# Performance work log

Hardware: AMD Instinct MI355X
Metric: run time of the kernel (lower is better)

Reference implementation:

```python
import jax, jax.numpy as jnp
import numpy as np

THRESHOLD_IOU = 0.8  # forward default in the original module


def setup_inputs() -> dict:
    key = jax.random.key(0)
    k1, k2, k3, k4 = jax.random.split(key, 4)
    N = M = 16
    H = W = 768
    # Binary masks (the original zeroes pixels to 0.0 and tests >0 via torch.where)
    masks_a = (jax.random.uniform(k1, (N, H, W)) > 0.6).astype(jnp.float32)
    masks_b = (jax.random.uniform(k2, (M, H, W)) > 0.6).astype(jnp.float32)
    # Make a few masks identical across labels so the IoU>threshold (suppression)
    # branch is exercised, not just the partial-overlap zeroing branch.
    masks_b = masks_b.at[:4].set(masks_a[:4])
    scores_a = jax.random.uniform(k3, (N,))
    scores_b = jax.random.uniform(k4, (M,))
    return {"masks_a": masks_a, "masks_b": masks_b,
            "scores_a": scores_a, "scores_b": scores_b}


def _overlap_filter(masks_a, masks_b, scores_a, scores_b, thr):
    # Sequential pairwise IoU + overlap zeroing, faithful to the original
    # nested product(enumerate(masks), enumerate(other_masks)) loop order
    # (i outer, j inner), where each pair sees masks already modified by
    # earlier pairs. Pruning ("keep") is applied after the loop; here it is
    # represented with static shapes as keep flags + zeroed-out rows.
    N, H, W = masks_a.shape
    M = masks_b.shape[0]
    P = H * W
    A0 = masks_a.reshape(N, P)
    B0 = masks_b.reshape(M, P)

    def body(carry, k):
        A, B, fi, fj = carry
        i = k // M
        j = k % M
        a = A[i]  # [P]
        b = B[j]  # [P]
        abin = a > 0
        bbin = b > 0
        inter = abin & bbin
        inter_sum = jnp.sum(inter.astype(jnp.float32))
        union_sum = jnp.sum((abin | bbin).astype(jnp.float32))
        iou = inter_sum / jnp.maximum(union_sum, 1.0)
        a_wins = scores_a[i] > scores_b[j]
        suppress = iou > thr                 # mark whole loser mask for removal
        zero_case = (iou > 0) & ~suppress    # zero overlapped pixels of loser
        b_new = jnp.where(zero_case & a_wins & inter, 0.0, b)
        a_new = jnp.where(zero_case & (~a_wins) & inter, 0.0, a)
        A = A.at[i].set(a_new)
        B = B.at[j].set(b_new)
        fj = fj.at[j].set(fj[j] | (suppress & a_wins))
        fi = fi.at[i].set(fi[i] | (suppress & ~a_wins))
        return (A, B, fi, fj), None

    fi0 = jnp.zeros(N, dtype=bool)
    fj0 = jnp.zeros(M, dtype=bool)
    (A, B, fi, fj), _ = jax.lax.scan(body, (A0, B0, fi0, fj0), jnp.arange(N * M))
    keep_a = ~fi
    keep_b = ~fj
    A = jnp.where(keep_a[:, None], A, 0.0)
    B = jnp.where(keep_b[:, None], B, 0.0)
    return A.reshape(N, H, W), B.reshape(M, H, W), keep_a, keep_b


def reference(masks_a, masks_b, scores_a, scores_b):
    return _overlap_filter(masks_a, masks_b, scores_a, scores_b, THRESHOLD_IOU)
```

## Files before the change

kernel.cpp:

```cpp
#include <hip/hip_runtime.h>
#include <stdint.h>

#define NM 16
#define HW_P 589824
#define U8PM 9216
#define F4PM 147456
#define F4PT 2359296
#define PT 512
#define NG 8

typedef unsigned long long u64;
typedef float vf4 __attribute__((ext_vector_type(4)));


__device__ __forceinline__ uint32_t spread4(uint32_t x) {
    uint32_t t = (x | (x << 12)) & 0x000F000Fu;
    t = (t | (t << 6)) & 0x03030303u;
    t = (t | (t << 3)) & 0x11111111u;
    return t;
}

__global__ __launch_bounds__(256) void binarize_kernel(
    const float* __restrict__ ma, const float* __restrict__ mb,
    uint32_t* __restrict__ bitsA, uint32_t* __restrict__ bitsB,
    int* __restrict__ meta)
{
    if (blockIdx.x == 0) meta[threadIdx.x] = 0;
    int g = blockIdx.x * 256 + threadIdx.x;
    int tensor = (g >= F4PT);
    int lg = tensor ? (g - F4PT) : g;
    const float* src = tensor ? mb : ma;
    vf4 v = __builtin_nontemporal_load(((const vf4*)src) + lg);
    unsigned long long q0 = __ballot(v.x > 0.0f);
    unsigned long long q1 = __ballot(v.y > 0.0f);
    unsigned long long q2 = __ballot(v.z > 0.0f);
    unsigned long long q3 = __ballot(v.w > 0.0f);
    int lane = threadIdx.x & 63;
    if (lane < 8) {
        uint32_t wd = spread4((uint32_t)(q0 >> (8 * lane)) & 0xFFu)
                    | (spread4((uint32_t)(q1 >> (8 * lane)) & 0xFFu) << 1)
                    | (spread4((uint32_t)(q2 >> (8 * lane)) & 0xFFu) << 2)
                    | (spread4((uint32_t)(q3 >> (8 * lane)) & 0xFFu) << 3);
        uint32_t* bits = tensor ? bitsB : bitsA;
        bits[((lg & ~63) >> 3) + lane] = wd;
    }
}

__global__ __launch_bounds__(PT, 1) void pipeline_kernel(
    const float* __restrict__ sa, const float* __restrict__ sb,
    uint32_t* bitsA, uint32_t* bitsB, int* meta, u64* msg)
{
    int* flagsA = meta + 32;
    int* flagsB = meta + 48;
    unsigned* cons = (unsigned*)(meta + 64);
    unsigned* prodflag = (unsigned*)(meta + 96);

    const int g = blockIdx.x;
    const int tid = threadIdx.x;
    const int wave = tid >> 6, lane = tid & 63;
    const int c0 = 2 * g, c1 = 2 * g + 1;

    __shared__ int part[8][4];
    __shared__ unsigned smeta_s;

    u64* A8 = (u64*)bitsA;
    u64* B8 = (u64*)bitsB;

    u64 a[18], b0[18], b1[18];

    const uint4* Bc0 = (const uint4*)(B8 + (size_t)c0 * U8PM);
    const uint4* Bc1 = (const uint4*)(B8 + (size_t)c1 * U8PM);
#pragma unroll
    for (int w = 0; w < 9; ++w) {
        uint4 q0 = Bc0[tid + PT * w];
        uint4 q1 = Bc1[tid + PT * w];
        b0[2 * w]     = ((u64)q0.y << 32) | q0.x;
        b0[2 * w + 1] = ((u64)q0.w << 32) | q0.z;
        b1[2 * w]     = ((u64)q1.y << 32) | q1.x;
        b1[2 * w + 1] = ((u64)q1.w << 32) | q1.z;
    }
    int v0 = 0, v1 = 0;
#pragma unroll
    for (int w = 0; w < 18; ++w) { v0 += __popcll(b0[w]); v1 += __popcll(b1[w]); }
#pragma unroll
    for (int off = 32; off >= 1; off >>= 1) {
        v0 += __shfl_xor(v0, off); v1 += __shfl_xor(v1, off);
    }
    if (lane == 0) { part[wave][0] = v0; part[wave][1] = v1; }
    __syncthreads();
    int pcb0 = 0, pcb1 = 0;
#pragma unroll
    for (int w = 0; w < 8; ++w) { pcb0 += part[wave ? 0 : 0][0], pcb0 = 0; break; }
    pcb0 = 0; pcb1 = 0;
#pragma unroll
    for (int w = 0; w < 8; ++w) { pcb0 += part[w][0]; pcb1 += part[w][1]; }
    if (g > 0 && tid == 64) {
        unsigned v;
        while (!(v = __hip_atomic_load(&prodflag[(g - 1) * 16 + 0],
                                       __ATOMIC_RELAXED, __HIP_MEMORY_SCOPE_AGENT))) {}
        smeta_s = v;
    }
    __syncthreads();
    unsigned mv = smeta_s;

    float sb0 = sb[c0], sb1 = sb[c1];
    int fb0 = 0, fb1 = 0;

    for (int t = 0; t < NM; ++t) {
        int pca, fa;
        if (g == 0) { pca = 0; fa = 0; }
        else { pca = (int)((mv >> 1) & 0xFFFFFu); fa = (int)((mv >> 21) & 1u); }

        if (g == 0) {
            const uint4* Ar = (const uint4*)(A8 + (size_t)t * U8PM);
#pragma unroll
            for (int w = 0; w < 9; ++w) {
                uint4 q = Ar[tid + PT * w];
                a[2 * w]     = ((u64)q.y << 32) | q.x;
                a[2 * w + 1] = ((u64)q.w << 32) | q.z;
            }
        } else {
            const u64* slot_in = msg + (size_t)((g - 1) * 4 + (t & 3)) * U8PM;
#pragma unroll
            for (int w = 0; w < 9; ++w) {
                int base = 2 * tid + 1024 * w;
                a[2 * w]     = __hip_atomic_load(&slot_in[base],
                                __ATOMIC_RELAXED, __HIP_MEMORY_SCOPE_AGENT);
                a[2 * w + 1] = __hip_atomic_load(&slot_in[base + 1],
                                __ATOMIC_RELAXED, __HIP_MEMORY_SCOPE_AGENT);
            }
        }

        int i0 = 0, i1 = 0, itr = 0, ipc = 0;
#pragma unroll
        for (int w = 0; w < 18; ++w) {
            u64 ab0 = a[w] & b0[w];
            i0 += __popcll(ab0);
            i1 += __popcll(a[w] & b1[w]);
            itr += __popcll(ab0 & b1[w]);
        }
        if (g == 0) {
#pragma unroll
            for (int w = 0; w < 18; ++w) ipc += __popcll(a[w]);
        }
#pragma unroll
        for (int off = 32; off >= 1; off >>= 1) {
            i0 += __shfl_xor(i0, off); i1 += __shfl_xor(i1, off);
            itr += __shfl_xor(itr, off); ipc += __shfl_xor(ipc, off);
        }
        if (lane == 0) {
            part[wave][0] = i0; part[wave][1] = i1;
            part[wave][2] = itr; part[wave][3] = ipc;
        }
        __syncthreads();
        if (g > 0 && tid == 67)
            __hip_atomic_store(&cons[g - 1], (unsigned)(t + 1),
                               __ATOMIC_RELAXED, __HIP_MEMORY_SCOPE_AGENT);
        int I0 = 0, I1 = 0, T = 0, PC = 0;
#pragma unroll
        for (int w = 0; w < 8; ++w) {
            I0 += part[w][0]; I1 += part[w][1];
            T  += part[w][2]; PC += part[w][3];
        }
        if (g == 0) pca = PC;

        float sai = sa[t];
        bool aupd = false;
        {
            int inter = I0;
            int uni = pca + pcb0 - inter;
            float iou = (float)inter / fmaxf((float)uni, 1.0f);
            bool aw = sai > sb0;
            if (iou > 0.8f) { if (aw) fb0 = 1; else fa = 1; }
            else if (inter > 0) {
                if (aw) {
                    pcb0 -= inter;
#pragma unroll
                    for (int w = 0; w < 18; ++w) b0[w] &= ~a[w];
                } else {
                    pca -= inter; aupd = true;
#pragma unroll
                    for (int w = 0; w < 18; ++w) a[w] &= ~b0[w];
                }
            }
        }
        {
            int inter = aupd ? (I1 - T) : I1;
            int uni = pca + pcb1 - inter;
            float iou = (float)inter / fmaxf((float)uni, 1.0f);
            bool aw = sai > sb1;
            if (iou > 0.8f) { if (aw) fb1 = 1; else fa = 1; }
            else if (inter > 0) {
                if (aw) {
                    pcb1 -= inter;
#pragma unroll
                    for (int w = 0; w < 18; ++w) b1[w] &= ~a[w];
                } else {
                    pca -= inter;
#pragma unroll
                    for (int w = 0; w < 18; ++w) a[w] &= ~b1[w];
                }
            }
        }

        if (g < NG - 1) {
            u64* slot_out = msg + (size_t)(g * 4 + (t & 3)) * U8PM;
#pragma unroll
            for (int w = 0; w < 9; ++w) {
                int base = 2 * tid + 1024 * w;
                __hip_atomic_store(&slot_out[base], a[2 * w],
                                   __ATOMIC_RELAXED, __HIP_MEMORY_SCOPE_AGENT);
                __hip_atomic_store(&slot_out[base + 1], a[2 * w + 1],
                                   __ATOMIC_RELAXED, __HIP_MEMORY_SCOPE_AGENT);
            }
        } else {
            uint4* Ar = (uint4*)(A8 + (size_t)t * U8PM);
#pragma unroll
            for (int w = 0; w < 9; ++w) {
                uint4 q;
                q.x = (uint32_t)a[2 * w];     q.y = (uint32_t)(a[2 * w] >> 32);
                q.z = (uint32_t)a[2 * w + 1]; q.w = (uint32_t)(a[2 * w + 1] >> 32);
                Ar[tid + PT * w] = q;
            }
            if (tid == 0) flagsA[t] = fa;
        }

        if (g > 0 && t + 1 < NM && tid == 64) {
            unsigned v;
            while (!(v = __hip_atomic_load(&prodflag[(g - 1) * 16 + t + 1],
                                           __ATOMIC_RELAXED, __HIP_MEMORY_SCOPE_AGENT))) {}
            smeta_s = v;
        }
        if (g < NG - 1 && t + 1 < NM && t + 1 >= 4 && tid == 65) {
            while (__hip_atomic_load(&cons[g], __ATOMIC_RELAXED,
                                     __HIP_MEMORY_SCOPE_AGENT) < (unsigned)(t - 2)) {}
        }
        __syncthreads();
        if (g < NG - 1 && tid == 0)
            __hip_atomic_store(&prodflag[g * 16 + t],
                               1u | ((unsigned)pca << 1) | ((unsigned)fa << 21),
                               __ATOMIC_RELAXED, __HIP_MEMORY_SCOPE_AGENT);
        mv = smeta_s;
    }

    uint4* Wc0 = (uint4*)(B8 + (size_t)c0 * U8PM);
    uint4* Wc1 = (uint4*)(B8 + (size_t)c1 * U8PM);
#pragma unroll
    for (int w = 0; w < 9; ++w) {
        uint4 q0, q1;
        q0.x = (uint32_t)b0[2 * w];     q0.y = (uint32_t)(b0[2 * w] >> 32);
        q0.z = (uint32_t)b0[2 * w + 1]; q0.w = (uint32_t)(b0[2 * w + 1] >> 32);
        q1.x = (uint32_t)b1[2 * w];     q1.y = (uint32_t)(b1[2 * w] >> 32);
        q1.z = (uint32_t)b1[2 * w + 1]; q1.w = (uint32_t)(b1[2 * w + 1] >> 32);
        Wc0[tid + PT * w] = q0;
        Wc1[tid + PT * w] = q1;
    }
    if (tid == 0) { flagsB[c0] = fb0; flagsB[c1] = fb1; }
}

__global__ __launch_bounds__(256) void expand_kernel(
    const uint32_t* __restrict__ bitsA, const uint32_t* __restrict__ bitsB,
    const int* __restrict__ meta, float* __restrict__ out)
{
    int g = blockIdx.x * 256 + threadIdx.x;
    int tensor = (g >= F4PT);
    int lg = tensor ? (g - F4PT) : g;
    const uint32_t* bits = tensor ? bitsB : bitsA;
    const int* flags = meta + (tensor ? 48 : 32);
    int m = lg / F4PM;
    bool keep = (flags[m] == 0);
    uint32_t wd = keep ? bits[lg >> 3] : 0u;
    int sh = (lg & 7) * 4;
    vf4 o;
    o.x = ((wd >> (sh + 0)) & 1u) ? 1.0f : 0.0f;
    o.y = ((wd >> (sh + 1)) & 1u) ? 1.0f : 0.0f;
    o.z = ((wd >> (sh + 2)) & 1u) ? 1.0f : 0.0f;
    o.w = ((wd >> (sh + 3)) & 1u) ? 1.0f : 0.0f;
    __builtin_nontemporal_store(o, ((vf4*)out) + g);
    if (g < 2 * NM) {
        const int* f = meta + 32;
        out[(size_t)2 * NM * HW_P + g] = f[g] ? 0.0f : 1.0f;
    }
}

extern "C" void kernel_launch(void* const* d_in, const int* in_sizes, int n_in,
                              void* d_out, int out_size, void* d_ws, size_t ws_size,
                              hipStream_t stream)
{
    const float* ma = (const float*)d_in[0];
    const float* mb = (const float*)d_in[1];
    const float* sa = (const float*)d_in[2];
    const float* sb = (const float*)d_in[3];
    float* out = (float*)d_out;
    char* ws = (char*)d_ws;

    uint32_t* bitsA = (uint32_t*)(ws);
    uint32_t* bitsB = (uint32_t*)(ws + 1179648);
    int* meta       = (int*)(ws + 2359296);
    u64* msg        = (u64*)(ws + 2360320);

    binarize_kernel<<<18432, 256, 0, stream>>>(ma, mb, bitsA, bitsB, meta);
    pipeline_kernel<<<NG, PT, 0, stream>>>(sa, sb, bitsA, bitsB, meta, msg);
    expand_kernel<<<18432, 256, 0, stream>>>(bitsA, bitsB, meta, out);
}
```

Baseline: 270.1 us.

## Fuse binarize, pipeline and expand into one persistent kernel with XCC-local pipeline

Merges the three launches into a single persistent 128-workgroup kernel. Every workgroup binarizes its slice, then a grid barrier runs, and the eight pipeline stages are picked from workgroups on the same XCC so that inter-stage messages stay in the shared L2. The other workgroups spin until the pipeline finishes, then all of them expand bits back to floats. This removes launch gaps and uses vectorized buffer loads with sc0 for message passing. The cost is that binarize and expand run on only 128 workgroups, and the kernel relies on all workgroups being co-resident and on spin barriers.

```diff
diff --git a/kernel.cpp b/kernel.cpp
--- a/kernel.cpp
+++ b/kernel.cpp
@@ -4,14 +4,30 @@
 #define NM 16
 #define HW_P 589824
 #define U8PM 9216
+#define C4PM 4608
 #define F4PM 147456
 #define F4PT 2359296
 #define PT 512
 #define NG 8
+#define NWG 128
+#define WGF4 36864
+#define ITERS 72
+#define MAGIC 0x51C0FFEEu
 
 typedef unsigned long long u64;
 typedef float vf4 __attribute__((ext_vector_type(4)));
-
+typedef int v4i __attribute__((ext_vector_type(4)));
+
+
+__device__ __forceinline__ unsigned aload(unsigned* p) {
+    return __hip_atomic_load(p, __ATOMIC_RELAXED, __HIP_MEMORY_SCOPE_AGENT);
+}
+__device__ __forceinline__ void astore(unsigned* p, unsigned v) {
+    __hip_atomic_store(p, v, __ATOMIC_RELAXED, __HIP_MEMORY_SCOPE_AGENT);
+}
+__device__ __forceinline__ unsigned afadd(unsigned* p, unsigned v) {
+    return __hip_atomic_fetch_add(p, v, __ATOMIC_RELAXED, __HIP_MEMORY_SCOPE_AGENT);
+}
 
 __device__ __forceinline__ uint32_t spread4(uint32_t x) {
     uint32_t t = (x | (x << 12)) & 0x000F000Fu;
@@ -20,266 +36,292 @@
     return t;
 }
 
-__global__ __launch_bounds__(256) void binarize_kernel(
+__device__ __forceinline__ uint4 load16_sc0(const void* base, int voff) {
+#if __has_builtin(__builtin_amdgcn_raw_buffer_load_v4f32)
+    union { unsigned u[4]; v4i v; } r;
+    r.u[0] = (unsigned)(uintptr_t)base;
+    r.u[1] = (unsigned)((uintptr_t)base >> 32);
+    r.u[2] = 0xFFFFFFFFu;
+    r.u[3] = 0x00020000u;
+    vf4 f = __builtin_amdgcn_raw_buffer_load_v4f32(r.v, voff, 0, 1 );
+    union { vf4 f; uint4 u; } c; c.f = f; return c.u;
+#else
+    const u64* p = (const u64*)((const char*)base + voff);
+    u64 lo = __hip_atomic_load((u64*)p,       __ATOMIC_RELAXED, __HIP_MEMORY_SCOPE_AGENT);
+    u64 hi = __hip_atomic_load((u64*)(p + 1), __ATOMIC_RELAXED, __HIP_MEMORY_SCOPE_AGENT);
+    uint4 q;
+    q.x = (uint32_t)lo; q.y = (uint32_t)(lo >> 32);
+    q.z = (uint32_t)hi; q.w = (uint32_t)(hi >> 32);
+    return q;
+#endif
+}
+
+__global__ __launch_bounds__(PT, 1) void fused_kernel(
     const float* __restrict__ ma, const float* __restrict__ mb,
-    uint32_t* __restrict__ bitsA, uint32_t* __restrict__ bitsB,
-    int* __restrict__ meta)
+    const float* __restrict__ sa, const float* __restrict__ sb,
+    uint32_t* bitsA, uint32_t* bitsB, int* meta, u64* msg, float* out)
 {
-    if (blockIdx.x == 0) meta[threadIdx.x] = 0;
-    int g = blockIdx.x * 256 + threadIdx.x;
-    int tensor = (g >= F4PT);
-    int lg = tensor ? (g - F4PT) : g;
-    const float* src = tensor ? mb : ma;
-    vf4 v = __builtin_nontemporal_load(((const vf4*)src) + lg);
-    unsigned long long q0 = __ballot(v.x > 0.0f);
-    unsigned long long q1 = __ballot(v.y > 0.0f);
-    unsigned long long q2 = __ballot(v.z > 0.0f);
-    unsigned long long q3 = __ballot(v.w > 0.0f);
-    int lane = threadIdx.x & 63;
-    if (lane < 8) {
-        uint32_t wd = spread4((uint32_t)(q0 >> (8 * lane)) & 0xFFu)
-                    | (spread4((uint32_t)(q1 >> (8 * lane)) & 0xFFu) << 1)
-                    | (spread4((uint32_t)(q2 >> (8 * lane)) & 0xFFu) << 2)
-                    | (spread4((uint32_t)(q3 >> (8 * lane)) & 0xFFu) << 3);
-        uint32_t* bits = tensor ? bitsB : bitsA;
-        bits[((lg & ~63) >> 3) + lane] = wd;
-    }
-}
-
-__global__ __launch_bounds__(PT, 1) void pipeline_kernel(
-    const float* __restrict__ sa, const float* __restrict__ sb,
-    uint32_t* bitsA, uint32_t* bitsB, int* meta, u64* msg)
-{
-    int* flagsA = meta + 32;
-    int* flagsB = meta + 48;
-    unsigned* cons = (unsigned*)(meta + 64);
-    unsigned* prodflag = (unsigned*)(meta + 96);
-
-    const int g = blockIdx.x;
-    const int tid = threadIdx.x;
+    const int wg = blockIdx.x, tid = threadIdx.x;
     const int wave = tid >> 6, lane = tid & 63;
-    const int c0 = 2 * g, c1 = 2 * g + 1;
+    unsigned* um = (unsigned*)meta;
+    unsigned* init_f = um;
+    unsigned* arrive = um + 1;
+    unsigned* pdone  = um + 2;
+    unsigned* cnt    = um + 8;
+    int* flagsA      = meta + 16;
+    int* flagsB      = meta + 32;
+    unsigned* cons   = um + 48;
+    unsigned* prodflag = um + 64;
 
     __shared__ int part[8][4];
     __shared__ unsigned smeta_s;
-
-    u64* A8 = (u64*)bitsA;
-    u64* B8 = (u64*)bitsB;
-
-    u64 a[18], b0[18], b1[18];
-
-    const uint4* Bc0 = (const uint4*)(B8 + (size_t)c0 * U8PM);
-    const uint4* Bc1 = (const uint4*)(B8 + (size_t)c1 * U8PM);
-#pragma unroll
-    for (int w = 0; w < 9; ++w) {
-        uint4 q0 = Bc0[tid + PT * w];
-        uint4 q1 = Bc1[tid + PT * w];
-        b0[2 * w]     = ((u64)q0.y << 32) | q0.x;
-        b0[2 * w + 1] = ((u64)q0.w << 32) | q0.z;
-        b1[2 * w]     = ((u64)q1.y << 32) | q1.x;
-        b1[2 * w + 1] = ((u64)q1.w << 32) | q1.z;
+    __shared__ int s_slot, s_winner;
+
+    const int tensor = (wg >= NWG / 2);
+    {
+        const float* src = tensor ? mb : ma;
+        uint32_t* bits = tensor ? bitsB : bitsA;
+        int lgbase = wg * WGF4 - (tensor ? F4PT : 0);
+        for (int it = 0; it < ITERS; ++it) {
+            int lg = lgbase + it * PT + tid;
+            vf4 v = __builtin_nontemporal_load(((const vf4*)src) + lg);
+            u64 q0 = __ballot(v.x > 0.0f);
+            u64 q1 = __ballot(v.y > 0.0f);
+            u64 q2 = __ballot(v.z > 0.0f);
+            u64 q3 = __ballot(v.w > 0.0f);
+            if (lane < 8) {
+                uint32_t wd = spread4((uint32_t)(q0 >> (8 * lane)) & 0xFFu)
+                            | (spread4((uint32_t)(q1 >> (8 * lane)) & 0xFFu) << 1)
+                            | (spread4((uint32_t)(q2 >> (8 * lane)) & 0xFFu) << 2)
+                            | (spread4((uint32_t)(q3 >> (8 * lane)) & 0xFFu) << 3);
+                bits[((lg & ~63) >> 3) + lane] = wd;
+            }
+        }
     }
-    int v0 = 0, v1 = 0;
-#pragma unroll
-    for (int w = 0; w < 18; ++w) { v0 += __popcll(b0[w]); v1 += __popcll(b1[w]); }
-#pragma unroll
-    for (int off = 32; off >= 1; off >>= 1) {
-        v0 += __shfl_xor(v0, off); v1 += __shfl_xor(v1, off);
-    }
-    if (lane == 0) { part[wave][0] = v0; part[wave][1] = v1; }
+    if (wg == 0 && tid >= 1 && tid < 256) astore(um + tid, 0u);
+    __threadfence();
     __syncthreads();
-    int pcb0 = 0, pcb1 = 0;
-#pragma unroll
-    for (int w = 0; w < 8; ++w) { pcb0 += part[wave ? 0 : 0][0], pcb0 = 0; break; }
-    pcb0 = 0; pcb1 = 0;
-#pragma unroll
-    for (int w = 0; w < 8; ++w) { pcb0 += part[w][0]; pcb1 += part[w][1]; }
-    if (g > 0 && tid == 64) {
-        unsigned v;
-        while (!(v = __hip_atomic_load(&prodflag[(g - 1) * 16 + 0],
-                                       __ATOMIC_RELAXED, __HIP_MEMORY_SCOPE_AGENT))) {}
-        smeta_s = v;
+    if (wg == 0 && tid == 0) astore(init_f, MAGIC);
+
+    int xcc;
+    asm volatile("s_getreg_b32 %0, hwreg(HW_REG_XCC_ID)" : "=s"(xcc));
+    xcc &= 7;
+    if (tid == 0) {
+        while (aload(init_f) != MAGIC) __builtin_amdgcn_s_sleep(2);
+        s_slot = (int)afadd(&cnt[xcc], 1u);
+        afadd(arrive, 1u);
+        while (aload(arrive) < NWG) __builtin_amdgcn_s_sleep(2);
+        int wnr = 0;
+        for (int x = 7; x >= 0; --x) if (aload(&cnt[x]) >= NG) wnr = x;
+        s_winner = wnr;
     }
     __syncthreads();
-    unsigned mv = smeta_s;
-
-    float sb0 = sb[c0], sb1 = sb[c1];
-    int fb0 = 0, fb1 = 0;
-
-    for (int t = 0; t < NM; ++t) {
-        int pca, fa;
-        if (g == 0) { pca = 0; fa = 0; }
-        else { pca = (int)((mv >> 1) & 0xFFFFFu); fa = (int)((mv >> 21) & 1u); }
-
-        if (g == 0) {
-            const uint4* Ar = (const uint4*)(A8 + (size_t)t * U8PM);
-#pragma unroll
-            for (int w = 0; w < 9; ++w) {
-                uint4 q = Ar[tid + PT * w];
-                a[2 * w]     = ((u64)q.y << 32) | q.x;
-                a[2 * w + 1] = ((u64)q.w << 32) | q.z;
-            }
-        } else {
-            const u64* slot_in = msg + (size_t)((g - 1) * 4 + (t & 3)) * U8PM;
-#pragma unroll
-            for (int w = 0; w < 9; ++w) {
-                int base = 2 * tid + 1024 * w;
-                a[2 * w]     = __hip_atomic_load(&slot_in[base],
-                                __ATOMIC_RELAXED, __HIP_MEMORY_SCOPE_AGENT);
-                a[2 * w + 1] = __hip_atomic_load(&slot_in[base + 1],
-                                __ATOMIC_RELAXED, __HIP_MEMORY_SCOPE_AGENT);
-            }
-        }
-
-        int i0 = 0, i1 = 0, itr = 0, ipc = 0;
-#pragma unroll
-        for (int w = 0; w < 18; ++w) {
-            u64 ab0 = a[w] & b0[w];
-            i0 += __popcll(ab0);
-            i1 += __popcll(a[w] & b1[w]);
-            itr += __popcll(ab0 & b1[w]);
-        }
-        if (g == 0) {
-#pragma unroll
-            for (int w = 0; w < 18; ++w) ipc += __popcll(a[w]);
+    __threadfence();
+    const bool participant = (xcc == s_winner) && (s_slot < NG);
+
+    if (participant) {
+        const int g = s_slot;
+        const int c0 = 2 * g, c1 = 2 * g + 1;
+        uint4* A4 = (uint4*)bitsA;
+        uint4* B4 = (uint4*)bitsB;
+        u64 a[18], b0[18], b1[18];
+
+        int v0 = 0, v1 = 0;
+#pragma unroll
+        for (int w = 0; w < 9; ++w) {
+            uint4 q0 = B4[(size_t)c0 * C4PM + tid + PT * w];
+            uint4 q1 = B4[(size_t)c1 * C4PM + tid + PT * w];
+            b0[2 * w] = ((u64)q0.y << 32) | q0.x; b0[2 * w + 1] = ((u64)q0.w << 32) | q0.z;
+            b1[2 * w] = ((u64)q1.y << 32) | q1.x; b1[2 * w + 1] = ((u64)q1.w << 32) | q1.z;
+            v0 += __popcll(b0[2 * w]) + __popcll(b0[2 * w + 1]);
+            v1 += __popcll(b1[2 * w]) + __popcll(b1[2 * w + 1]);
         }
 #pragma unroll
         for (int off = 32; off >= 1; off >>= 1) {
-            i0 += __shfl_xor(i0, off); i1 += __shfl_xor(i1, off);
-            itr += __shfl_xor(itr, off); ipc += __shfl_xor(ipc, off);
-        }
-        if (lane == 0) {
-            part[wave][0] = i0; part[wave][1] = i1;
-            part[wave][2] = itr; part[wave][3] = ipc;
-        }
+            v0 += __shfl_xor(v0, off); v1 += __shfl_xor(v1, off);
+        }
+        if (lane == 0) { part[wave][0] = v0; part[wave][1] = v1; }
         __syncthreads();
-        if (g > 0 && tid == 67)
-            __hip_atomic_store(&cons[g - 1], (unsigned)(t + 1),
-                               __ATOMIC_RELAXED, __HIP_MEMORY_SCOPE_AGENT);
-        int I0 = 0, I1 = 0, T = 0, PC = 0;
-#pragma unroll
-        for (int w = 0; w < 8; ++w) {
-            I0 += part[w][0]; I1 += part[w][1];
-            T  += part[w][2]; PC += part[w][3];
-        }
-        if (g == 0) pca = PC;
-
-        float sai = sa[t];
-        bool aupd = false;
-        {
-            int inter = I0;
-            int uni = pca + pcb0 - inter;
-            float iou = (float)inter / fmaxf((float)uni, 1.0f);
-            bool aw = sai > sb0;
-            if (iou > 0.8f) { if (aw) fb0 = 1; else fa = 1; }
-            else if (inter > 0) {
-                if (aw) {
-                    pcb0 -= inter;
-#pragma unroll
-                    for (int w = 0; w < 18; ++w) b0[w] &= ~a[w];
-                } else {
-                    pca -= inter; aupd = true;
-#pragma unroll
-                    for (int w = 0; w < 18; ++w) a[w] &= ~b0[w];
-                }
-            }
-        }
-        {
-            int inter = aupd ? (I1 - T) : I1;
-            int uni = pca + pcb1 - inter;
-            float iou = (float)inter / fmaxf((float)uni, 1.0f);
-            bool aw = sai > sb1;
-            if (iou > 0.8f) { if (aw) fb1 = 1; else fa = 1; }
-            else if (inter > 0) {
-                if (aw) {
-                    pcb1 -= inter;
-#pragma unroll
-                    for (int w = 0; w < 18; ++w) b1[w] &= ~a[w];
-                } else {
-                    pca -= inter;
-#pragma unroll
-                    for (int w = 0; w < 18; ++w) a[w] &= ~b1[w];
-                }
-            }
-        }
-
-        if (g < NG - 1) {
-            u64* slot_out = msg + (size_t)(g * 4 + (t & 3)) * U8PM;
-#pragma unroll
-            for (int w = 0; w < 9; ++w) {
-                int base = 2 * tid + 1024 * w;
-                __hip_atomic_store(&slot_out[base], a[2 * w],
-                                   __ATOMIC_RELAXED, __HIP_MEMORY_SCOPE_AGENT);
-                __hip_atomic_store(&slot_out[base + 1], a[2 * w + 1],
-                                   __ATOMIC_RELAXED, __HIP_MEMORY_SCOPE_AGENT);
-            }
-        } else {
-            uint4* Ar = (uint4*)(A8 + (size_t)t * U8PM);
-#pragma unroll
-            for (int w = 0; w < 9; ++w) {
-                uint4 q;
-                q.x = (uint32_t)a[2 * w];     q.y = (uint32_t)(a[2 * w] >> 32);
-                q.z = (uint32_t)a[2 * w + 1]; q.w = (uint32_t)(a[2 * w + 1] >> 32);
-                Ar[tid + PT * w] = q;
-            }
-            if (tid == 0) flagsA[t] = fa;
-        }
-
-        if (g > 0 && t + 1 < NM && tid == 64) {
-            unsigned v;
-            while (!(v = __hip_atomic_load(&prodflag[(g - 1) * 16 + t + 1],
-                                           __ATOMIC_RELAXED, __HIP_MEMORY_SCOPE_AGENT))) {}
-            smeta_s = v;
-        }
-        if (g < NG - 1 && t + 1 < NM && t + 1 >= 4 && tid == 65) {
-            while (__hip_atomic_load(&cons[g], __ATOMIC_RELAXED,
-                                     __HIP_MEMORY_SCOPE_AGENT) < (unsigned)(t - 2)) {}
-        }
+        int pcb0 = 0, pcb1 = 0;
+#pragma unroll
+        for (int w = 0; w < 8; ++w) { pcb0 += part[w][0]; pcb1 += part[w][1]; }
         __syncthreads();
-        if (g < NG - 1 && tid == 0)
-            __hip_atomic_store(&prodflag[g * 16 + t],
-                               1u | ((unsigned)pca << 1) | ((unsigned)fa << 21),
-                               __ATOMIC_RELAXED, __HIP_MEMORY_SCOPE_AGENT);
-        mv = smeta_s;
+        float sb0 = sb[c0], sb1 = sb[c1];
+        int fb0 = 0, fb1 = 0;
+
+        for (int t = 0; t < NM; ++t) {
+            if (g > 0 && tid == 0) {
+                unsigned v;
+                while (!(v = aload(&prodflag[(g - 1) * 16 + t]))) {}
+                smeta_s = v;
+            }
+            if (g < NG - 1 && t >= 4 && tid == 64) {
+                while (aload(&cons[g]) < (unsigned)(t - 3)) {}
+            }
+            __syncthreads();
+
+            int pca, fa;
+            if (g == 0) {
+                pca = 0; fa = 0;
+#pragma unroll
+                for (int w = 0; w < 9; ++w) {
+                    uint4 q = A4[(size_t)t * C4PM + tid + PT * w];
+                    a[2 * w] = ((u64)q.y << 32) | q.x;
+                    a[2 * w + 1] = ((u64)q.w << 32) | q.z;
+                }
+            } else {
+                unsigned mv = smeta_s;
+                pca = (int)((mv >> 1) & 0xFFFFFu);
+                fa  = (int)((mv >> 21) & 1u);
+                const char* slot_in =
+                    (const char*)(msg + (size_t)((g - 1) * 4 + (t & 3)) * U8PM);
+#pragma unroll
+                for (int w = 0; w < 9; ++w) {
+                    uint4 q = load16_sc0(slot_in, tid * 16 + w * 8192);
+                    a[2 * w] = ((u64)q.y << 32) | q.x;
+                    a[2 * w + 1] = ((u64)q.w << 32) | q.z;
+                }
+            }
+
+            int i0 = 0, i1 = 0, itr = 0, ipc = 0;
+#pragma unroll
+            for (int w = 0; w < 18; ++w) {
+                u64 ab0 = a[w] & b0[w];
+                i0 += __popcll(ab0);
+                i1 += __popcll(a[w] & b1[w]);
+                itr += __popcll(ab0 & b1[w]);
+            }
+            if (g == 0) {
+#pragma unroll
+                for (int w = 0; w < 18; ++w) ipc += __popcll(a[w]);
+            }
+#pragma unroll
+            for (int off = 32; off >= 1; off >>= 1) {
+                i0 += __shfl_xor(i0, off); i1 += __shfl_xor(i1, off);
+                itr += __shfl_xor(itr, off); ipc += __shfl_xor(ipc, off);
+            }
+            if (lane == 0) {
+                part[wave][0] = i0; part[wave][1] = i1;
+                part[wave][2] = itr; part[wave][3] = ipc;
+            }
+            __syncthreads();
+            if (g > 0 && tid == 65)
+                astore(&cons[g - 1], (unsigned)(t + 1));
+            int I0 = 0, I1 = 0, T = 0, PC = 0;
+#pragma unroll
+            for (int w = 0; w < 8; ++w) {
+                I0 += part[w][0]; I1 += part[w][1];
+                T  += part[w][2]; PC += part[w][3];
+            }
+            if (g == 0) pca = PC;
+
+            float sai = sa[t];
+            bool aupd = false;
+            {
+                int inter = I0;
+                int uni = pca + pcb0 - inter;
+                float iou = (float)inter / fmaxf((float)uni, 1.0f);
+                bool aw = sai > sb0;
+                if (iou > 0.8f) { if (aw) fb0 = 1; else fa = 1; }
+                else if (inter > 0) {
+                    if (aw) {
+                        pcb0 -= inter;
+#pragma unroll
+                        for (int w = 0; w < 18; ++w) b0[w] &= ~a[w];
+                    } else {
+                        pca -= inter; aupd = true;
+#pragma unroll
+                        for (int w = 0; w < 18; ++w) a[w] &= ~b0[w];
+                    }
+                }
+            }
+            {
+                int inter = aupd ? (I1 - T) : I1;
+                int uni = pca + pcb1 - inter;
+                float iou = (float)inter / fmaxf((float)uni, 1.0f);
+                bool aw = sai > sb1;
+                if (iou > 0.8f) { if (aw) fb1 = 1; else fa = 1; }
+                else if (inter > 0) {
+                    if (aw) {
+                        pcb1 -= inter;
+#pragma unroll
+                        for (int w = 0; w < 18; ++w) b1[w] &= ~a[w];
+                    } else {
+                        pca -= inter;
+#pragma unroll
+                        for (int w = 0; w < 18; ++w) a[w] &= ~b1[w];
+                    }
+                }
+            }
+
+            if (g < NG - 1) {
+                uint4* so = (uint4*)(msg + (size_t)(g * 4 + (t & 3)) * U8PM);
+#pragma unroll
+                for (int w = 0; w < 9; ++w) {
+                    uint4 q;
+                    q.x = (uint32_t)a[2 * w];     q.y = (uint32_t)(a[2 * w] >> 32);
+                    q.z = (uint32_t)a[2 * w + 1]; q.w = (uint32_t)(a[2 * w + 1] >> 32);
+                    so[tid + PT * w] = q;
+                }
+                __threadfence_block();
+                __syncthreads();
+                if (tid == 0)
+                    astore(&prodflag[g * 16 + t],
+                           1u | ((unsigned)pca << 1) | ((unsigned)fa << 21));
+            } else {
+                uint4* Ar = A4 + (size_t)t * C4PM;
+#pragma unroll
+                for (int w = 0; w < 9; ++w) {
+                    uint4 q;
+                    q.x = (uint32_t)a[2 * w];     q.y = (uint32_t)(a[2 * w] >> 32);
+                    q.z = (uint32_t)a[2 * w + 1]; q.w = (uint32_t)(a[2 * w + 1] >> 32);
+                    Ar[tid + PT * w] = q;
+                }
+                if (tid == 0) flagsA[t] = fa;
+                __syncthreads();
+            }
+        }
+
+        uint4* Wc0 = B4 + (size_t)c0 * C4PM;
+        uint4* Wc1 = B4 + (size_t)c1 * C4PM;
+#pragma unroll
+        for (int w = 0; w < 9; ++w) {
+            uint4 q0, q1;
+            q0.x = (uint32_t)b0[2 * w];     q0.y = (uint32_t)(b0[2 * w] >> 32);
+            q0.z = (uint32_t)b0[2 * w + 1]; q0.w = (uint32_t)(b0[2 * w + 1] >> 32);
+            q1.x = (uint32_t)b1[2 * w];     q1.y = (uint32_t)(b1[2 * w] >> 32);
+            q1.z = (uint32_t)b1[2 * w + 1]; q1.w = (uint32_t)(b1[2 * w + 1] >> 32);
+            Wc0[tid + PT * w] = q0;
+            Wc1[tid + PT * w] = q1;
+        }
+        if (tid == 0) { flagsB[c0] = fb0; flagsB[c1] = fb1; }
+        __threadfence();
+        __syncthreads();
+        if (tid == 0) afadd(pdone, 1u);
     }
 
-    uint4* Wc0 = (uint4*)(B8 + (size_t)c0 * U8PM);
-    uint4* Wc1 = (uint4*)(B8 + (size_t)c1 * U8PM);
-#pragma unroll
-    for (int w = 0; w < 9; ++w) {
-        uint4 q0, q1;
-        q0.x = (uint32_t)b0[2 * w];     q0.y = (uint32_t)(b0[2 * w] >> 32);
-        q0.z = (uint32_t)b0[2 * w + 1]; q0.w = (uint32_t)(b0[2 * w + 1] >> 32);
-        q1.x = (uint32_t)b1[2 * w];     q1.y = (uint32_t)(b1[2 * w] >> 32);
-        q1.z = (uint32_t)b1[2 * w + 1]; q1.w = (uint32_t)(b1[2 * w + 1] >> 32);
-        Wc0[tid + PT * w] = q0;
-        Wc1[tid + PT * w] = q1;
-    }
-    if (tid == 0) { flagsB[c0] = fb0; flagsB[c1] = fb1; }
-}
-
-__global__ __launch_bounds__(256) void expand_kernel(
-    const uint32_t* __restrict__ bitsA, const uint32_t* __restrict__ bitsB,
-    const int* __restrict__ meta, float* __restrict__ out)
-{
-    int g = blockIdx.x * 256 + threadIdx.x;
-    int tensor = (g >= F4PT);
-    int lg = tensor ? (g - F4PT) : g;
-    const uint32_t* bits = tensor ? bitsB : bitsA;
-    const int* flags = meta + (tensor ? 48 : 32);
-    int m = lg / F4PM;
-    bool keep = (flags[m] == 0);
-    uint32_t wd = keep ? bits[lg >> 3] : 0u;
-    int sh = (lg & 7) * 4;
-    vf4 o;
-    o.x = ((wd >> (sh + 0)) & 1u) ? 1.0f : 0.0f;
-    o.y = ((wd >> (sh + 1)) & 1u) ? 1.0f : 0.0f;
-    o.z = ((wd >> (sh + 2)) & 1u) ? 1.0f : 0.0f;
-    o.w = ((wd >> (sh + 3)) & 1u) ? 1.0f : 0.0f;
-    __builtin_nontemporal_store(o, ((vf4*)out) + g);
-    if (g < 2 * NM) {
-        const int* f = meta + 32;
-        out[(size_t)2 * NM * HW_P + g] = f[g] ? 0.0f : 1.0f;
+    if (tid == 0) { while (aload(pdone) < NG) __builtin_amdgcn_s_sleep(2); }
+    __syncthreads();
+    __threadfence();
+    {
+        const uint32_t* bits = tensor ? bitsB : bitsA;
+        const int* flags = meta + (tensor ? 32 : 16);
+        int lgbase = wg * WGF4 - (tensor ? F4PT : 0);
+        for (int it = 0; it < ITERS; ++it) {
+            int lg = lgbase + it * PT + tid;
+            int m = lg / F4PM;
+            bool keep = (flags[m] == 0);
+            uint32_t wd = keep ? bits[lg >> 3] : 0u;
+            int sh = (lg & 7) * 4;
+            vf4 o;
+            o.x = ((wd >> (sh + 0)) & 1u) ? 1.0f : 0.0f;
+            o.y = ((wd >> (sh + 1)) & 1u) ? 1.0f : 0.0f;
+            o.z = ((wd >> (sh + 2)) & 1u) ? 1.0f : 0.0f;
+            o.w = ((wd >> (sh + 3)) & 1u) ? 1.0f : 0.0f;
+            __builtin_nontemporal_store(o, ((vf4*)out) + (tensor ? lg + F4PT : lg));
+        }
+        if (wg == 0 && tid < 2 * NM)
+            out[(size_t)2 * NM * HW_P + tid] = meta[16 + tid] ? 0.0f : 1.0f;
     }
 }
 
@@ -299,7 +341,6 @@
     int* meta       = (int*)(ws + 2359296);
     u64* msg        = (u64*)(ws + 2360320);
 
-    binarize_kernel<<<18432, 256, 0, stream>>>(ma, mb, bitsA, bitsB, meta);
-    pipeline_kernel<<<NG, PT, 0, stream>>>(sa, sb, bitsA, bitsB, meta, msg);
-    expand_kernel<<<18432, 256, 0, stream>>>(bitsA, bitsB, meta, out);
-}
+    fused_kernel<<<NWG, PT, 0, stream>>>(ma, mb, sa, sb,
+                                         bitsA, bitsB, meta, msg, out);
+}
```

After: 349.6 us. 29.5% more time.
